# Optimization experiments

Hardware: AMD Instinct MI355X
Metric: run time of the kernel (lower is better)

The kernel has to match this reference:

```python
import jax, jax.numpy as jnp
import numpy as np
from jax import lax

BATCH = 2560
N_CLS = 128    # QP decision dim n
N_INEQ = 128   # number of inequality constraints
N_FEAT = 128
IPM_ITERS = 20
SIGMA = 0.1    # centering parameter


def setup_inputs() -> dict:
    key = jax.random.key(0)
    k1, k2, k3, k4, k5 = jax.random.split(key, 5)
    x = jax.random.normal(k1, (BATCH, N_FEAT), dtype=jnp.float32)
    # symmetric positive-definite Q (qpth requires PD Q)
    A = jax.random.normal(k2, (N_CLS, N_CLS), dtype=jnp.float32) / np.sqrt(N_CLS).astype(np.float32)
    Q = A @ A.T + 1e-4 * jnp.eye(N_CLS, dtype=jnp.float32)
    p = jax.random.normal(k3, (BATCH, N_CLS), dtype=jnp.float32)
    G = jax.random.uniform(k4, (N_INEQ, N_CLS), minval=-1.0, maxval=1.0, dtype=jnp.float32)
    # h > 0 so z = 0 is strictly feasible -> well-conditioned IPM
    h = jax.random.uniform(k5, (N_INEQ,), dtype=jnp.float32) + 1.0
    return {"x": x, "Q": Q, "p": p, "G": G, "h": h, "m": 1}


def _qp_solve(Q, p, G, h, iters=IPM_ITERS, sigma=SIGMA):
    """Batched primal-dual interior-point solve of
       min_z 1/2 z'Qz + p'z  s.t.  Gz + s = h, s >= 0.
    Q: [n,n] shared; p: [B,n]; G: [m,n] shared; h: [m] shared."""
    B, n = p.shape
    mI = G.shape[0]
    z = jnp.zeros((B, n), p.dtype)
    s = jnp.ones((B, mI), p.dtype)
    lam = jnp.ones((B, mI), p.dtype)
    GT = G.T

    def frac_to_boundary(v, dv):
        safe = jnp.where(dv < 0, dv, -1.0)
        r = jnp.where(dv < 0, -v / safe, 1e9)
        return jnp.minimum(1.0, 0.99 * jnp.min(r, axis=1, keepdims=True))

    def step(carry, _):
        z, s, lam = carry
        r_d = z @ Q.T + p + lam @ G          # [B,n]  Qz + p + G'lam
        r_p = z @ GT + s - h                 # [B,m]  Gz + s - h
        mu = jnp.mean(s * lam, axis=1, keepdims=True)
        r_c = s * lam - sigma * mu           # [B,m]
        d = lam / s                          # [B,m]
        # reduced KKT: (Q + G' D G) dz = -r_d + G'((r_c - lam*r_p)/s)
        M = Q[None] + jnp.einsum('ki,bk,kj->bij', G, d, G)  # [B,n,n]
        rhs = -r_d + ((r_c - lam * r_p) / s) @ G             # [B,n]
        dz = jnp.linalg.solve(M, rhs[..., None])[..., 0]
        ds = -r_p - dz @ GT
        dlam = (-r_c - lam * ds) / s
        a = jnp.minimum(frac_to_boundary(s, ds), frac_to_boundary(lam, dlam))
        return (z + a * dz, s + a * ds, lam + a * dlam), None

    (z, s, lam), _ = lax.scan(step, (z, s, lam), None, length=iters)
    return z


def reference(x, Q, p, G, h, m):
    # m==1 path of OptNet.forward: p stays [B,n], Q shared [n,n]
    pf = p.T if m > 1 else p
    z = _qp_solve(Q.astype(jnp.float32), pf.astype(jnp.float32),
                  G.astype(jnp.float32), h.astype(jnp.float32))
    out = z.reshape(10, -1)  # faithful to x.view(10, -1)
    return jax.nn.log_softmax(out, axis=1)
```

## Files before the change

kernel.cpp:

```cpp
#include <hip/hip_runtime.h>
#include <math.h>


#define B_TOT 2560
#define TB 32
#define NB (B_TOT/TB)

__device__ __forceinline__ int ROFF(int i){ return (i*(i+1))>>1; }
__device__ __forceinline__ int rowStart(int i){
  int a=i>>2, b=i&3;
  return ((a+1)*((a<<1)+b))<<2;
}
#define TRI_SZ 8448

__device__ __forceinline__ int rowOfIdx(int idx){
  int i = (int)((sqrtf(8.f*(float)idx+1.f)-1.f)*0.5f);
  while (((i+1)*(i+2)>>1) <= idx) ++i;
  while (((i*(i+1))>>1) > idx) --i;
  return i;
}

__device__ __forceinline__ void chol_diag_gj(float* tri, int c0, int lane){
  float rowA[16], rowW[16];
  const int r = lane;
  #pragma unroll
  for (int j=0;j<16;++j){ rowA[j]=0.f; rowW[j]=0.f; }
  if (r < 16){
    const float* src = &tri[rowStart(c0+r)+c0];
    #pragma unroll
    for (int q=0;q<4;++q){
      if (q <= (r>>2)){
        float4 w = *(const float4*)&src[4*q];
        rowA[4*q+0]=w.x; rowA[4*q+1]=w.y; rowA[4*q+2]=w.z; rowA[4*q+3]=w.w;
      }
    }
    #pragma unroll
    for (int j=0;j<16;++j) if (j>r) rowA[j]=0.f;
    #pragma unroll
    for (int j=0;j<16;++j) rowW[j] = (j==r)?1.f:0.f;
  }
  #pragma unroll
  for (int k=0;k<16;++k){
    float akk = __shfl(rowA[k], k, 64);
    akk = fmaxf(akk, 1e-12f);
    float linv = rsqrtf(akk);
    float lrk = rowA[k]*linv;
    if (r==k){
      #pragma unroll
      for (int c=0;c<16;++c) rowW[c] *= linv;
    }
    #pragma unroll
    for (int j=k+1;j<16;++j){
      float ljk = __shfl(lrk, j, 64);
      if (r>=j) rowA[j] = fmaf(-lrk, ljk, rowA[j]);
    }
    #pragma unroll
    for (int c=0;c<=k;++c){
      float wkc = __shfl(rowW[c], k, 64);
      if (r>k) rowW[c] = fmaf(-lrk, wkc, rowW[c]);
    }
  }
  if (r < 16){
    float* dst = &tri[rowStart(c0+r)+c0];
    #pragma unroll
    for (int q=0;q<4;++q){
      if (q <= (r>>2)){
        float4 w; w.x=rowW[4*q+0]; w.y=rowW[4*q+1]; w.z=rowW[4*q+2]; w.w=rowW[4*q+3];
        *(float4*)&dst[4*q] = w;
      }
    }
  }
}

__device__ __forceinline__ void trail_tile8(float* tri, int pc0, int i0, int j0,
                                            bool diag){
  float4 Pi[8][4], Pj[8][4];
  #pragma unroll
  for (int ii=0;ii<8;++ii){
    const float* rp = &tri[rowStart(i0+ii)+pc0];
    #pragma unroll
    for (int q=0;q<4;++q) Pi[ii][q] = *(const float4*)&rp[4*q];
  }
  #pragma unroll
  for (int jj=0;jj<8;++jj){
    const float* rp = &tri[rowStart(j0+jj)+pc0];
    #pragma unroll
    for (int q=0;q<4;++q) Pj[jj][q] = *(const float4*)&rp[4*q];
  }
  float acc[8][8];
  #pragma unroll
  for (int ii=0;ii<8;++ii)
    #pragma unroll
    for (int jj=0;jj<8;++jj) acc[ii][jj]=0.f;
  #pragma unroll
  for (int q=0;q<4;++q){
    #pragma unroll
    for (int ii=0;ii<8;++ii){
      #pragma unroll
      for (int jj=0;jj<8;++jj){
        acc[ii][jj] = fmaf(Pi[ii][q].x, Pj[jj][q].x, acc[ii][jj]);
        acc[ii][jj] = fmaf(Pi[ii][q].y, Pj[jj][q].y, acc[ii][jj]);
        acc[ii][jj] = fmaf(Pi[ii][q].z, Pj[jj][q].z, acc[ii][jj]);
        acc[ii][jj] = fmaf(Pi[ii][q].w, Pj[jj][q].w, acc[ii][jj]);
      }
    }
  }
  if (!diag){
    #pragma unroll
    for (int ii=0;ii<8;++ii){
      float4* p = (float4*)&tri[rowStart(i0+ii)+j0];
      float4 v0=p[0], v1=p[1];
      v0.x-=acc[ii][0]; v0.y-=acc[ii][1]; v0.z-=acc[ii][2]; v0.w-=acc[ii][3];
      v1.x-=acc[ii][4]; v1.y-=acc[ii][5]; v1.z-=acc[ii][6]; v1.w-=acc[ii][7];
      p[0]=v0; p[1]=v1;
    }
  } else {
    #pragma unroll
    for (int ii=0;ii<8;++ii){
      float4* p = (float4*)&tri[rowStart(i0+ii)+j0];
      const int nq = (ii>>2)+1;
      #pragma unroll
      for (int q=0;q<2;++q){
        if (q<nq){
          float4 v=p[q];
          v.x-=acc[ii][4*q+0]; v.y-=acc[ii][4*q+1];
          v.z-=acc[ii][4*q+2]; v.w-=acc[ii][4*q+3];
          p[q]=v;
        }
      }
    }
  }
}

__device__ __forceinline__ void trail_tile4(float* tri, int pc0, int i0, int j0){
  float4 Pi[4][4], Pj[4][4];
  #pragma unroll
  for (int ii=0;ii<4;++ii){
    const float* rp = &tri[rowStart(i0+ii)+pc0];
    #pragma unroll
    for (int q=0;q<4;++q) Pi[ii][q] = *(const float4*)&rp[4*q];
  }
  #pragma unroll
  for (int jj=0;jj<4;++jj){
    const float* rp = &tri[rowStart(j0+jj)+pc0];
    #pragma unroll
    for (int q=0;q<4;++q) Pj[jj][q] = *(const float4*)&rp[4*q];
  }
  float acc[4][4];
  #pragma unroll
  for (int ii=0;ii<4;++ii)
    #pragma unroll
    for (int jj=0;jj<4;++jj) acc[ii][jj]=0.f;
  #pragma unroll
  for (int q=0;q<4;++q){
    #pragma unroll
    for (int ii=0;ii<4;++ii){
      #pragma unroll
      for (int jj=0;jj<4;++jj){
        acc[ii][jj] = fmaf(Pi[ii][q].x, Pj[jj][q].x, acc[ii][jj]);
        acc[ii][jj] = fmaf(Pi[ii][q].y, Pj[jj][q].y, acc[ii][jj]);
        acc[ii][jj] = fmaf(Pi[ii][q].z, Pj[jj][q].z, acc[ii][jj]);
        acc[ii][jj] = fmaf(Pi[ii][q].w, Pj[jj][q].w, acc[ii][jj]);
      }
    }
  }
  #pragma unroll
  for (int ii=0;ii<4;++ii){
    float4* p = (float4*)&tri[rowStart(i0+ii)+j0];
    float4 v=p[0];
    v.x-=acc[ii][0]; v.y-=acc[ii][1]; v.z-=acc[ii][2]; v.w-=acc[ii][3];
    p[0]=v;
  }
}

__device__ __forceinline__ void panel_row(float* tri, int c0, int r){
  const int rb = rowStart(r)+c0;
  float a[16];
  #pragma unroll
  for (int q=0;q<4;++q){
    float4 w = *(const float4*)&tri[rb+4*q];
    a[4*q+0]=w.x; a[4*q+1]=w.y; a[4*q+2]=w.z; a[4*q+3]=w.w;
  }
  float x[16];
  #pragma unroll
  for (int c=0;c<16;++c){
    float acc=0.f;
    const int lb = rowStart(c0+c)+c0;
    #pragma unroll
    for (int q=0;q<=(c>>2);++q){
      float4 w = *(const float4*)&tri[lb+4*q];
      if (4*q+0<=c) acc = fmaf(w.x, a[4*q+0], acc);
      if (4*q+1<=c) acc = fmaf(w.y, a[4*q+1], acc);
      if (4*q+2<=c) acc = fmaf(w.z, a[4*q+2], acc);
      if (4*q+3<=c) acc = fmaf(w.w, a[4*q+3], acc);
    }
    x[c]=acc;
  }
  #pragma unroll
  for (int q=0;q<4;++q){
    float4 w; w.x=x[4*q+0]; w.y=x[4*q+1]; w.z=x[4*q+2]; w.w=x[4*q+3];
    *(float4*)&tri[rb+4*q] = w;
  }
}

__device__ void chol_factor(float* tri, int t, int lane, int wid){
  for (int kb=0; kb<8; ++kb){
    const int c0 = kb*16;
    if (wid==(kb&3)) chol_diag_gj(tri, c0, lane);
    __syncthreads();
    const int rem = 112 - c0;
    if (t < rem) panel_row(tri, c0, c0+16+t);
    __syncthreads();
    if (rem > 0){
      const int base = c0+16;
      const int T = rem>>3;
      const int ntile = (T*(T+1))>>1;
      for (int idx=t; idx<ntile; idx+=256){
        int I = rowOfIdx(idx);
        int J = idx - ROFF(I);
        trail_tile8(tri, c0, base+8*I, base+8*J, I==J);
      }
    }
    __syncthreads();
  }
}

__device__ void chol_factor_w2(float* tri, int t, int lane, int wid){
  for (int kb=0; kb<8; ++kb){
    const int c0 = kb*16;
    if (wid==0) chol_diag_gj(tri, c0, lane);
    __syncthreads();
    const int rem = 112 - c0;
    if (t < rem) panel_row(tri, c0, c0+16+t);
    __syncthreads();
    if (rem > 0){
      const int base = c0+16;
      const int R = rem>>2;
      const int ntile = (R*(R+1))>>1;
      for (int idx=t; idx<ntile; idx+=128){
        int I = rowOfIdx(idx);
        int J = idx - ROFF(I);
        trail_tile4(tri, c0, base+4*I, base+4*J);
      }
    }
    __syncthreads();
  }
}

__device__ void tri_solve_w2(const float* tri, float* rhs, int t){
  for (int kb=0;kb<8;++kb){
    const int c0=kb*16;
    if (t<16){
      const int c=t;
      const float* lrow = &tri[rowStart(c0+c)+c0];
      float acc=0.f;
      #pragma unroll
      for (int cp=0;cp<16;++cp) if (cp<=c) acc = fmaf(lrow[cp], rhs[c0+cp], acc);
      rhs[c0+c] = acc;
    }
    __syncthreads();
    const int rem = 112-c0;
    if (t<rem){
      const int r = c0+16+t;
      const int rb = rowStart(r)+c0;
      float acc = rhs[r];
      #pragma unroll
      for (int q=0;q<4;++q){
        float4 w = *(const float4*)&tri[rb+4*q];
        acc = fmaf(-w.x, rhs[c0+4*q+0], acc);
        acc = fmaf(-w.y, rhs[c0+4*q+1], acc);
        acc = fmaf(-w.z, rhs[c0+4*q+2], acc);
        acc = fmaf(-w.w, rhs[c0+4*q+3], acc);
      }
      rhs[r] = acc;
    }
    __syncthreads();
  }
  for (int kb=7;kb>=0;--kb){
    const int c0=kb*16;
    if (t<16){
      const int c=t;
      float acc=0.f;
      #pragma unroll
      for (int cp=0;cp<16;++cp)
        if (cp>=c) acc = fmaf(tri[rowStart(c0+cp)+c0+c], rhs[c0+cp], acc);
      rhs[c0+c] = acc;
    }
    __syncthreads();
    if (t<c0){
      float acc = rhs[t];
      #pragma unroll
      for (int c=0;c<16;++c) acc = fmaf(-tri[rowStart(c0+c)+t], rhs[c0+c], acc);
      rhs[t]=acc;
    }
    __syncthreads();
  }
}

__global__ __launch_bounds__(256) void k_prepA(const float* __restrict__ Q,
                                               float* __restrict__ TRIQ){
  __shared__ __align__(16) float tri[TRI_SZ];
  const int t = threadIdx.x;
  const int lane = t&63, wid = t>>6;
  for (int idx=t; idx<8256; idx+=256){
    int i = rowOfIdx(idx); int j = idx - ROFF(i);
    tri[rowStart(i)+j] = Q[i*128+j];
  }
  __syncthreads();
  chol_factor(tri, t, lane, wid);
  for (int idx=t; idx<TRI_SZ; idx+=256) TRIQ[idx]=tri[idx];
}

__global__ __launch_bounds__(256) void k_prepB(const float* __restrict__ TRIQ,
        const float* __restrict__ Gm, float* __restrict__ Qi, float* __restrict__ M1)
{
  __shared__ __align__(16) float tri[TRI_SZ];
  __shared__ float Xl[128*32];
  const int t = threadIdx.x, cc = blockIdx.x;
  const int a0 = (cc&3)*32;
  const bool ident = (cc<4);
  for (int idx=t; idx<TRI_SZ; idx+=256) tri[idx]=TRIQ[idx];
  for (int idx=t; idx<4096; idx+=256){
    int i=idx>>5, j=idx&31;
    Xl[idx] = ident ? ((i==(a0+j))?1.f:0.f) : Gm[(a0+j)*128+i];
  }
  __syncthreads();
  for (int kb=0;kb<8;++kb){
    const int c0=kb*16;
    if (t<32){
      float v[16], x[16];
      #pragma unroll
      for (int c=0;c<16;++c) v[c]=Xl[(c0+c)*32+t];
      #pragma unroll
      for (int c=0;c<16;++c){
        float acc=0.f;
        const int lb=rowStart(c0+c)+c0;
        #pragma unroll
        for (int cp=0;cp<16;++cp) if (cp<=c) acc=fmaf(tri[lb+cp], v[cp], acc);
        x[c]=acc;
      }
      #pragma unroll
      for (int c=0;c<16;++c) Xl[(c0+c)*32+t]=x[c];
    }
    __syncthreads();
    const int rem=112-c0;
    for (int rr=(t>>5); rr<rem; rr+=8){
      const int r=c0+16+rr, j=t&31;
      float acc=Xl[r*32+j];
      #pragma unroll
      for (int c=0;c<16;++c) acc = fmaf(-tri[rowStart(r)+c0+c], Xl[(c0+c)*32+j], acc);
      Xl[r*32+j]=acc;
    }
    __syncthreads();
  }
  for (int kb=7;kb>=0;--kb){
    const int c0=kb*16;
    if (t<32){
      float v[16], x[16];
      #pragma unroll
      for (int c=0;c<16;++c) v[c]=Xl[(c0+c)*32+t];
      #pragma unroll
      for (int c=0;c<16;++c){
        float acc=0.f;
        #pragma unroll
        for (int cp=0;cp<16;++cp) if (cp>=c) acc=fmaf(tri[rowStart(c0+cp)+c0+c], v[cp], acc);
        x[c]=acc;
      }
      #pragma unroll
      for (int c=0;c<16;++c) Xl[(c0+c)*32+t]=x[c];
    }
    __syncthreads();
    for (int rr=(t>>5); rr<c0; rr+=8){
      const int j=t&31;
      float acc=Xl[rr*32+j];
      #pragma unroll
      for (int c=0;c<16;++c) acc = fmaf(-tri[rowStart(c0+c)+rr], Xl[(c0+c)*32+j], acc);
      Xl[rr*32+j]=acc;
    }
    __syncthreads();
  }
  float* dst = ident ? Qi : M1;
  for (int idx=t; idx<4096; idx+=256){
    int i=idx>>5, j=idx&31;
    dst[i*128+a0+j] = Xl[idx];
  }
}

__global__ __launch_bounds__(256) void k_kmat(const float* __restrict__ Gm,
        const float* __restrict__ M1, float* __restrict__ K, float* __restrict__ Kd){
  const int idx = blockIdx.x*256 + threadIdx.x;
  const int a = idx>>7, bcol = idx&127;
  float a0=0.f,a1=0.f,a2=0.f,a3=0.f;
  #pragma unroll
  for (int j=0;j<128;j+=4){
    a0 = fmaf(Gm[a*128+j+0], M1[(j+0)*128+bcol], a0);
    a1 = fmaf(Gm[a*128+j+1], M1[(j+1)*128+bcol], a1);
    a2 = fmaf(Gm[a*128+j+2], M1[(j+2)*128+bcol], a2);
    a3 = fmaf(Gm[a*128+j+3], M1[(j+3)*128+bcol], a3);
  }
  float acc = (a0+a1)+(a2+a3);
  K[idx] = acc;
  if (a==bcol) Kd[a]=acc;
}

__global__ __launch_bounds__(256) void k_init(const float* __restrict__ p,
    float* __restrict__ Pt, float* __restrict__ S, float* __restrict__ LAM,
    float* __restrict__ GZ, float* __restrict__ QZ, float* __restrict__ Zst){
  int idx = blockIdx.x*256 + threadIdx.x;
  if (idx < 128*B_TOT){
    int i = idx/B_TOT, b = idx - i*B_TOT;
    Pt[idx] = p[b*128+i];
    S[idx]=1.f; LAM[idx]=1.f; GZ[idx]=0.f; QZ[idx]=0.f; Zst[idx]=0.f;
  }
}

__global__ __launch_bounds__(256) void k_B(const float* __restrict__ G,
    const float* __restrict__ M1, const float* __restrict__ Pt,
    const float* __restrict__ h,
    const float* __restrict__ S, const float* __restrict__ LAM,
    const float* __restrict__ GZ, const float* __restrict__ QZ,
    float* __restrict__ RHS, float* __restrict__ TV){
  __shared__ float wm_l[128*33];
  __shared__ float rhs_l[128*33];
  __shared__ float part_l[8*33];
  __shared__ float mu_l[TB];
  __shared__ float h_l[128];
  const int t=threadIdx.x, g=t>>5, bl=t&31;
  const int b = blockIdx.x*TB + bl;
  if (t<128) h_l[t]=h[t];
  __syncthreads();
  float sv[16], lv[16], rpv[16];
  float prod=0.f;
  #pragma unroll
  for (int q=0;q<16;++q){
    int i = g + 8*q;
    float s = S[i*B_TOT+b], l = LAM[i*B_TOT+b], gz = GZ[i*B_TOT+b];
    sv[q]=s; lv[q]=l; rpv[q]=gz+s-h_l[i];
    prod += s*l;
  }
  part_l[g*33+bl] = prod;
  __syncthreads();
  if (g==0){
    float m=0.f;
    #pragma unroll
    for (int q=0;q<8;++q) m += part_l[q*33+bl];
    mu_l[bl] = m*(1.f/128.f);
  }
  __syncthreads();
  const float mu = mu_l[bl];
  #pragma unroll
  for (int q=0;q<16;++q){
    int i=g+8*q;
    float rc = sv[q]*lv[q] - 0.1f*mu;
    wm_l[i*33+bl] = (rc - lv[q]*rpv[q])/sv[q] - lv[q];
  }
  __syncthreads();
  const int r0 = g*16;
  float acc[16];
  #pragma unroll
  for (int q=0;q<16;++q) acc[q] = -(QZ[(r0+q)*B_TOT+b] + Pt[(r0+q)*B_TOT+b]);
  #pragma unroll 2
  for (int j=0;j<128;++j){
    float wmv = wm_l[j*33+bl];
    const float4* gp = (const float4*)&G[j*128+r0];
    #pragma unroll
    for (int q4=0;q4<4;++q4){
      float4 gv = gp[q4];
      acc[4*q4+0]=fmaf(gv.x,wmv,acc[4*q4+0]);
      acc[4*q4+1]=fmaf(gv.y,wmv,acc[4*q4+1]);
      acc[4*q4+2]=fmaf(gv.z,wmv,acc[4*q4+2]);
      acc[4*q4+3]=fmaf(gv.w,wmv,acc[4*q4+3]);
    }
  }
  #pragma unroll
  for (int q=0;q<16;++q){
    rhs_l[(r0+q)*33+bl]=acc[q];
    RHS[(r0+q)*B_TOT+b]=acc[q];
  }
  __syncthreads();
  #pragma unroll
  for (int q=0;q<16;++q) acc[q]=0.f;
  #pragma unroll 2
  for (int j=0;j<128;++j){
    float rv = rhs_l[j*33+bl];
    const float4* mp = (const float4*)&M1[j*128+r0];
    #pragma unroll
    for (int q4=0;q4<4;++q4){
      float4 mv = mp[q4];
      acc[4*q4+0]=fmaf(mv.x,rv,acc[4*q4+0]);
      acc[4*q4+1]=fmaf(mv.y,rv,acc[4*q4+1]);
      acc[4*q4+2]=fmaf(mv.z,rv,acc[4*q4+2]);
      acc[4*q4+3]=fmaf(mv.w,rv,acc[4*q4+3]);
    }
  }
  #pragma unroll
  for (int q=0;q<16;++q) TV[(r0+q)*B_TOT+b]=acc[q];
}

__global__ __launch_bounds__(128) void k_C(const float* __restrict__ K,
    const float* __restrict__ Kd, const float* __restrict__ h,
    const float* __restrict__ TV,
    float* __restrict__ S, float* __restrict__ LAM, float* __restrict__ GZ,
    float* __restrict__ Y, float* __restrict__ ALPHA){
  __shared__ __align__(16) float tri[TRI_SZ];
  __shared__ float scl_l[128];
  __shared__ float sh_t[128];
  __shared__ float red[2];
  const int t = threadIdx.x, b = blockIdx.x;
  const int lane = t&63, wid = t>>6;
  float s_t=S[t*B_TOT+b], l_t=LAM[t*B_TOT+b], g_t=GZ[t*B_TOT+b];
  float rp_t = g_t + s_t - h[t];
  float prod = s_t*l_t;
  #pragma unroll
  for (int o=32;o>0;o>>=1) prod += __shfl_xor(prod,o,64);
  if (lane==0) red[wid]=prod;
  __syncthreads();
  const float mu = (red[0]+red[1])*(1.f/128.f);
  float rc_t = s_t*l_t - 0.1f*mu;
  float di_t = fminf(s_t/l_t, 1e30f);
  float sc_t = rsqrtf(Kd[t]+di_t);
  scl_l[t]=sc_t;
  sh_t[t]=TV[t*B_TOT+b]*sc_t;
  __syncthreads();
  #pragma unroll 4
  for (int i=0;i<128;++i){
    if (t<=i) tri[rowStart(i)+t] = (t==i)?1.f : K[i*128+t]*scl_l[i]*sc_t;
  }
  __syncthreads();
  chol_factor_w2(tri, t, lane, wid);
  tri_solve_w2(tri, sh_t, t);
  float y = sh_t[t]*sc_t;
  float gd = di_t*y;
  float ds = -rp_t - gd;
  float dl = (-rc_t - l_t*ds)/s_t;
  float ra = 1e9f;
  if (ds<0.f) ra = -s_t/ds;
  if (dl<0.f) ra = fminf(ra,-l_t/dl);
  #pragma unroll
  for (int o=32;o>0;o>>=1) ra = fminf(ra,__shfl_xor(ra,o,64));
  __syncthreads();
  if (lane==0) red[wid]=ra;
  __syncthreads();
  const float alpha = fminf(1.0f, 0.99f*fminf(red[0],red[1]));
  S[t*B_TOT+b]   = s_t + alpha*ds;
  LAM[t*B_TOT+b] = l_t + alpha*dl;
  GZ[t*B_TOT+b]  = g_t + alpha*gd;
  Y[t*B_TOT+b]   = y;
  if (t==0) ALPHA[b]=alpha;
}

__global__ __launch_bounds__(256) void k_DB(const float* __restrict__ G,
    const float* __restrict__ Qi, const float* __restrict__ M1,
    const float* __restrict__ Pt, const float* __restrict__ h,
    const float* __restrict__ S, const float* __restrict__ LAM,
    const float* __restrict__ GZ,
    const float* __restrict__ Y, const float* __restrict__ ALPHA,
    float* __restrict__ Zst, float* __restrict__ QZ,
    float* __restrict__ RHS, float* __restrict__ TV){
  __shared__ float bufA[128*33];
  __shared__ float bufB[128*33];
  __shared__ float part_l[8*33];
  __shared__ float mu_l[TB];
  __shared__ float h_l[128];
  const int t=threadIdx.x, g=t>>5, bl=t&31;
  const int b = blockIdx.x*TB + bl;
  const int r0 = g*16;
  if (t<128) h_l[t]=h[t];
  #pragma unroll
  for (int q=0;q<16;++q){
    int i=g+8*q;
    bufA[i*33+bl] = Y[i*B_TOT+b];
  }
  const float alpha = ALPHA[b];
  __syncthreads();
  float acc[16];
  #pragma unroll
  for (int q=0;q<16;++q) acc[q]=RHS[(r0+q)*B_TOT+b];
  #pragma unroll 2
  for (int j=0;j<128;++j){
    float yv = bufA[j*33+bl];
    const float4* gp=(const float4*)&G[j*128+r0];
    #pragma unroll
    for (int q4=0;q4<4;++q4){
      float4 gv=gp[q4];
      acc[4*q4+0]=fmaf(-gv.x,yv,acc[4*q4+0]);
      acc[4*q4+1]=fmaf(-gv.y,yv,acc[4*q4+1]);
      acc[4*q4+2]=fmaf(-gv.z,yv,acc[4*q4+2]);
      acc[4*q4+3]=fmaf(-gv.w,yv,acc[4*q4+3]);
    }
  }
  __syncthreads();
  #pragma unroll
  for (int q=0;q<16;++q){
    const int i=r0+q;
    float qz_new = QZ[i*B_TOT+b] + alpha*acc[q];
    QZ[i*B_TOT+b] = qz_new;
    bufB[i*33+bl] = acc[q];
    bufA[i*33+bl] = qz_new;
  }
  __syncthreads();
  #pragma unroll
  for (int q=0;q<16;++q) acc[q]=0.f;
  #pragma unroll 2
  for (int j=0;j<128;++j){
    float vv = bufB[j*33+bl];
    const float4* qp4=(const float4*)&Qi[j*128+r0];
    #pragma unroll
    for (int q4=0;q4<4;++q4){
      float4 qv=qp4[q4];
      acc[4*q4+0]=fmaf(qv.x,vv,acc[4*q4+0]);
      acc[4*q4+1]=fmaf(qv.y,vv,acc[4*q4+1]);
      acc[4*q4+2]=fmaf(qv.z,vv,acc[4*q4+2]);
      acc[4*q4+3]=fmaf(qv.w,vv,acc[4*q4+3]);
    }
  }
  #pragma unroll
  for (int q=0;q<16;++q){
    float* zp=&Zst[(r0+q)*B_TOT+b];
    *zp = *zp + alpha*acc[q];
  }
  __syncthreads();
  float sv[16], lv[16], rpv[16];
  float prod=0.f;
  #pragma unroll
  for (int q=0;q<16;++q){
    int i = g + 8*q;
    float s = S[i*B_TOT+b], l = LAM[i*B_TOT+b], gz = GZ[i*B_TOT+b];
    sv[q]=s; lv[q]=l; rpv[q]=gz+s-h_l[i];
    prod += s*l;
  }
  part_l[g*33+bl] = prod;
  __syncthreads();
  if (g==0){
    float m=0.f;
    #pragma unroll
    for (int q=0;q<8;++q) m += part_l[q*33+bl];
    mu_l[bl] = m*(1.f/128.f);
  }
  __syncthreads();
  const float mu = mu_l[bl];
  #pragma unroll
  for (int q=0;q<16;++q){
    int i=g+8*q;
    float rc = sv[q]*lv[q] - 0.1f*mu;
    bufB[i*33+bl] = (rc - lv[q]*rpv[q])/sv[q] - lv[q];
  }
  __syncthreads();
  #pragma unroll
  for (int q=0;q<16;++q) acc[q] = -(bufA[(r0+q)*33+bl] + Pt[(r0+q)*B_TOT+b]);
  #pragma unroll 2
  for (int j=0;j<128;++j){
    float wmv = bufB[j*33+bl];
    const float4* gp = (const float4*)&G[j*128+r0];
    #pragma unroll
    for (int q4=0;q4<4;++q4){
      float4 gv = gp[q4];
      acc[4*q4+0]=fmaf(gv.x,wmv,acc[4*q4+0]);
      acc[4*q4+1]=fmaf(gv.y,wmv,acc[4*q4+1]);
      acc[4*q4+2]=fmaf(gv.z,wmv,acc[4*q4+2]);
      acc[4*q4+3]=fmaf(gv.w,wmv,acc[4*q4+3]);
    }
  }
  __syncthreads();
  #pragma unroll
  for (int q=0;q<16;++q){
    RHS[(r0+q)*B_TOT+b]=acc[q];
    bufA[(r0+q)*33+bl]=acc[q];
  }
  __syncthreads();
  #pragma unroll
  for (int q=0;q<16;++q) acc[q]=0.f;
  #pragma unroll 2
  for (int j=0;j<128;++j){
    float rv = bufA[j*33+bl];
    const float4* mp = (const float4*)&M1[j*128+r0];
    #pragma unroll
    for (int q4=0;q4<4;++q4){
      float4 mv = mp[q4];
      acc[4*q4+0]=fmaf(mv.x,rv,acc[4*q4+0]);
      acc[4*q4+1]=fmaf(mv.y,rv,acc[4*q4+1]);
      acc[4*q4+2]=fmaf(mv.z,rv,acc[4*q4+2]);
      acc[4*q4+3]=fmaf(mv.w,rv,acc[4*q4+3]);
    }
  }
  #pragma unroll
  for (int q=0;q<16;++q) TV[(r0+q)*B_TOT+b]=acc[q];
}

__global__ __launch_bounds__(256) void k_D(const float* __restrict__ G,
    const float* __restrict__ Qi, const float* __restrict__ RHS,
    const float* __restrict__ Y, const float* __restrict__ ALPHA,
    float* __restrict__ Zst, float* __restrict__ QZ){
  __shared__ float y_l[128*33];
  __shared__ float v_l[128*33];
  const int t=threadIdx.x, g=t>>5, bl=t&31;
  const int b = blockIdx.x*TB + bl;
  #pragma unroll
  for (int q=0;q<16;++q){
    int i=g+8*q;
    y_l[i*33+bl] = Y[i*B_TOT+b];
  }
  const float alpha = ALPHA[b];
  __syncthreads();
  const int r0=g*16;
  float acc[16];
  #pragma unroll
  for (int q=0;q<16;++q) acc[q]=RHS[(r0+q)*B_TOT+b];
  #pragma unroll 2
  for (int j=0;j<128;++j){
    float yv = y_l[j*33+bl];
    const float4* gp=(const float4*)&G[j*128+r0];
    #pragma unroll
    for (int q4=0;q4<4;++q4){
      float4 gv=gp[q4];
      acc[4*q4+0]=fmaf(-gv.x,yv,acc[4*q4+0]);
      acc[4*q4+1]=fmaf(-gv.y,yv,acc[4*q4+1]);
      acc[4*q4+2]=fmaf(-gv.z,yv,acc[4*q4+2]);
      acc[4*q4+3]=fmaf(-gv.w,yv,acc[4*q4+3]);
    }
  }
  #pragma unroll
  for (int q=0;q<16;++q){
    v_l[(r0+q)*33+bl]=acc[q];
    float* qp=&QZ[(r0+q)*B_TOT+b];
    *qp = *qp + alpha*acc[q];
  }
  __syncthreads();
  #pragma unroll
  for (int q=0;q<16;++q) acc[q]=0.f;
  #pragma unroll 2
  for (int j=0;j<128;++j){
    float vv = v_l[j*33+bl];
    const float4* qp4=(const float4*)&Qi[j*128+r0];
    #pragma unroll
    for (int q4=0;q4<4;++q4){
      float4 qv=qp4[q4];
      acc[4*q4+0]=fmaf(qv.x,vv,acc[4*q4+0]);
      acc[4*q4+1]=fmaf(qv.y,vv,acc[4*q4+1]);
      acc[4*q4+2]=fmaf(qv.z,vv,acc[4*q4+2]);
      acc[4*q4+3]=fmaf(qv.w,vv,acc[4*q4+3]);
    }
  }
  #pragma unroll
  for (int q=0;q<16;++q){
    float* zp=&Zst[(r0+q)*B_TOT+b];
    *zp = *zp + alpha*acc[q];
  }
}

__global__ __launch_bounds__(1024) void k_logsoftmax(const float* __restrict__ Zst,
                                                     float* __restrict__ out){
  __shared__ float red[16];
  __shared__ float sval[2];
  const int r = blockIdx.x, t = threadIdx.x;
  float m = -1e30f;
  for (int k=t;k<32768;k+=1024){
    float v = Zst[(k&127)*B_TOT + r*256 + (k>>7)];
    m = fmaxf(m, v);
  }
  #pragma unroll
  for (int o=32;o>0;o>>=1) m = fmaxf(m, __shfl_down(m,o,64));
  if ((t&63)==0) red[t>>6] = m;
  __syncthreads();
  if (t==0){ float mm=red[0]; for (int w=1;w<16;++w) mm=fmaxf(mm,red[w]); sval[0]=mm; }
  __syncthreads();
  const float mx = sval[0];
  float s=0.f;
  for (int k=t;k<32768;k+=1024){
    float v = Zst[(k&127)*B_TOT + r*256 + (k>>7)];
    s += expf(v-mx);
  }
  #pragma unroll
  for (int o=32;o>0;o>>=1) s += __shfl_down(s,o,64);
  if ((t&63)==0) red[t>>6]=s;
  __syncthreads();
  if (t==0){ float ss=0.f; for (int w=0;w<16;++w) ss+=red[w]; sval[1]=logf(ss); }
  __syncthreads();
  const float lse = sval[1];
  for (int k=t;k<32768;k+=1024){
    float v = Zst[(k&127)*B_TOT + r*256 + (k>>7)];
    out[(size_t)r*32768+k] = v-mx-lse;
  }
}

extern "C" void kernel_launch(void* const* d_in, const int* in_sizes, int n_in,
                              void* d_out, int out_size, void* d_ws, size_t ws_size,
                              hipStream_t stream){
  const float* Q = (const float*)d_in[1];
  const float* p = (const float*)d_in[2];
  const float* G = (const float*)d_in[3];
  const float* h = (const float*)d_in[4];
  float* ws  = (float*)d_ws;
  const int NE = 128*B_TOT;
  float* Zst = ws;
  float* Qi  = Zst + NE;
  float* M1  = Qi + 16384;
  float* K   = M1 + 16384;
  float* Kd  = K + 16384;
  float* ALPHA = Kd + 128;
  float* Pt  = ALPHA + 2560;
  float* S   = Pt + NE;
  float* LAM = S + NE;
  float* GZ  = LAM + NE;
  float* QZ  = GZ + NE;
  float* RHS = QZ + NE;
  float* TV  = RHS + NE;
  float* Y   = TV + NE;
  float* TRIQ= Y + NE;
  float* out = (float*)d_out;

  hipLaunchKernelGGL(k_prepA, dim3(1), dim3(256), 0, stream, Q, TRIQ);
  hipLaunchKernelGGL(k_prepB, dim3(8), dim3(256), 0, stream, TRIQ, G, Qi, M1);
  hipLaunchKernelGGL(k_kmat, dim3(64), dim3(256), 0, stream, G, M1, K, Kd);
  hipLaunchKernelGGL(k_init, dim3((NE+255)/256), dim3(256), 0, stream,
                     p, Pt, S, LAM, GZ, QZ, Zst);
  hipLaunchKernelGGL(k_B, dim3(NB), dim3(256), 0, stream,
                     G, M1, Pt, h, S, LAM, GZ, QZ, RHS, TV);
  for (int it=0; it<20; ++it){
    hipLaunchKernelGGL(k_C, dim3(B_TOT), dim3(128), 0, stream,
                       K, Kd, h, TV, S, LAM, GZ, Y, ALPHA);
    if (it < 19){
      hipLaunchKernelGGL(k_DB, dim3(NB), dim3(256), 0, stream,
                         G, Qi, M1, Pt, h, S, LAM, GZ, Y, ALPHA,
                         Zst, QZ, RHS, TV);
    } else {
      hipLaunchKernelGGL(k_D, dim3(NB), dim3(256), 0, stream,
                         G, Qi, RHS, Y, ALPHA, Zst, QZ);
    }
  }
  hipLaunchKernelGGL(k_logsoftmax, dim3(10), dim3(1024), 0, stream, Zst, out);
}
```

Measured before the change: 8.089 ms.

## Use 192 threads in Cholesky kernel with contiguous tile ranges and Pi reuse

```diff
diff --git a/kernel.cpp b/kernel.cpp
--- a/kernel.cpp
+++ b/kernel.cpp
@@ -5,6 +5,7 @@
 #define B_TOT 2560
 #define TB 32
 #define NB (B_TOT/TB)
+#define NTC 192
 
 __device__ __forceinline__ int ROFF(int i){ return (i*(i+1))>>1; }
 __device__ __forceinline__ int rowStart(int i){
@@ -132,14 +133,10 @@
   }
 }
 
-__device__ __forceinline__ void trail_tile4(float* tri, int pc0, int i0, int j0){
-  float4 Pi[4][4], Pj[4][4];
-  #pragma unroll
-  for (int ii=0;ii<4;++ii){
-    const float* rp = &tri[rowStart(i0+ii)+pc0];
-    #pragma unroll
-    for (int q=0;q<4;++q) Pi[ii][q] = *(const float4*)&rp[4*q];
-  }
+__device__ __forceinline__ void trail_tile4_pi(float* tri, int pc0,
+                                               const float4 Pi[4][4],
+                                               int i0, int j0){
+  float4 Pj[4][4];
   #pragma unroll
   for (int jj=0;jj<4;++jj){
     const float* rp = &tri[rowStart(j0+jj)+pc0];
@@ -170,6 +167,16 @@
     float4 v=p[0];
     v.x-=acc[ii][0]; v.y-=acc[ii][1]; v.z-=acc[ii][2]; v.w-=acc[ii][3];
     p[0]=v;
+  }
+}
+
+__device__ __forceinline__ void load_pi4(const float* tri, int pc0, int i0,
+                                         float4 Pi[4][4]){
+  #pragma unroll
+  for (int ii=0;ii<4;++ii){
+    const float* rp = &tri[rowStart(i0+ii)+pc0];
+    #pragma unroll
+    for (int q=0;q<4;++q) Pi[ii][q] = *(const float4*)&rp[4*q];
   }
 }
 
@@ -225,7 +232,7 @@
   }
 }
 
-__device__ void chol_factor_w2(float* tri, int t, int lane, int wid){
+__device__ void chol_factor_w3(float* tri, int t, int lane, int wid){
   for (int kb=0; kb<8; ++kb){
     const int c0 = kb*16;
     if (wid==0) chol_diag_gj(tri, c0, lane);
@@ -235,12 +242,25 @@
     __syncthreads();
     if (rem > 0){
       const int base = c0+16;
-      const int R = rem>>2;
-      const int ntile = (R*(R+1))>>1;
-      for (int idx=t; idx<ntile; idx+=128){
-        int I = rowOfIdx(idx);
-        int J = idx - ROFF(I);
-        trail_tile4(tri, c0, base+4*I, base+4*J);
+      const int T = rem>>2;
+      const int ntile = (T*(T+1))>>1;
+      const int lo = (ntile*t)/NTC;
+      const int hi = (ntile*(t+1))/NTC;
+      if (lo < hi){
+        int I = rowOfIdx(lo);
+        int nextRow = ROFF(I+1);
+        float4 Pi[4][4];
+        load_pi4(tri, c0, base+4*I, Pi);
+        for (int idx=lo; idx<hi; ++idx){
+          if (idx >= nextRow){
+            ++I;
+            while (idx >= ROFF(I+1)) ++I;
+            nextRow = ROFF(I+1);
+            load_pi4(tri, c0, base+4*I, Pi);
+          }
+          const int J = idx - ROFF(I);
+          trail_tile4_pi(tri, c0, Pi, base+4*I, base+4*J);
+        }
       }
     }
     __syncthreads();
@@ -497,7 +517,7 @@
   for (int q=0;q<16;++q) TV[(r0+q)*B_TOT+b]=acc[q];
 }
 
-__global__ __launch_bounds__(128) void k_C(const float* __restrict__ K,
+__global__ __launch_bounds__(NTC) void k_C(const float* __restrict__ K,
     const float* __restrict__ Kd, const float* __restrict__ h,
     const float* __restrict__ TV,
     float* __restrict__ S, float* __restrict__ LAM, float* __restrict__ GZ,
@@ -505,47 +525,59 @@
   __shared__ __align__(16) float tri[TRI_SZ];
   __shared__ float scl_l[128];
   __shared__ float sh_t[128];
-  __shared__ float red[2];
+  __shared__ float red[3];
   const int t = threadIdx.x, b = blockIdx.x;
   const int lane = t&63, wid = t>>6;
-  float s_t=S[t*B_TOT+b], l_t=LAM[t*B_TOT+b], g_t=GZ[t*B_TOT+b];
-  float rp_t = g_t + s_t - h[t];
-  float prod = s_t*l_t;
+  float s_t=0.f,l_t=0.f,g_t=0.f,rp_t=0.f;
+  float prod = 0.f;
+  if (t<128){
+    s_t=S[t*B_TOT+b]; l_t=LAM[t*B_TOT+b]; g_t=GZ[t*B_TOT+b];
+    rp_t = g_t + s_t - h[t];
+    prod = s_t*l_t;
+  }
   #pragma unroll
   for (int o=32;o>0;o>>=1) prod += __shfl_xor(prod,o,64);
   if (lane==0) red[wid]=prod;
   __syncthreads();
-  const float mu = (red[0]+red[1])*(1.f/128.f);
-  float rc_t = s_t*l_t - 0.1f*mu;
-  float di_t = fminf(s_t/l_t, 1e30f);
-  float sc_t = rsqrtf(Kd[t]+di_t);
-  scl_l[t]=sc_t;
-  sh_t[t]=TV[t*B_TOT+b]*sc_t;
+  const float mu = (red[0]+red[1]+red[2])*(1.f/128.f);
+  float rc_t=0.f, di_t=0.f, sc_t=0.f;
+  if (t<128){
+    rc_t = s_t*l_t - 0.1f*mu;
+    di_t = fminf(s_t/l_t, 1e30f);
+    sc_t = rsqrtf(Kd[t]+di_t);
+    scl_l[t]=sc_t;
+    sh_t[t]=TV[t*B_TOT+b]*sc_t;
+  }
   __syncthreads();
   #pragma unroll 4
   for (int i=0;i<128;++i){
     if (t<=i) tri[rowStart(i)+t] = (t==i)?1.f : K[i*128+t]*scl_l[i]*sc_t;
   }
   __syncthreads();
-  chol_factor_w2(tri, t, lane, wid);
+  chol_factor_w3(tri, t, lane, wid);
   tri_solve_w2(tri, sh_t, t);
-  float y = sh_t[t]*sc_t;
-  float gd = di_t*y;
-  float ds = -rp_t - gd;
-  float dl = (-rc_t - l_t*ds)/s_t;
+  float y=0.f, gd=0.f, ds=0.f, dl=0.f;
   float ra = 1e9f;
-  if (ds<0.f) ra = -s_t/ds;
-  if (dl<0.f) ra = fminf(ra,-l_t/dl);
+  if (t<128){
+    y = sh_t[t]*sc_t;
+    gd = di_t*y;
+    ds = -rp_t - gd;
+    dl = (-rc_t - l_t*ds)/s_t;
+    if (ds<0.f) ra = -s_t/ds;
+    if (dl<0.f) ra = fminf(ra,-l_t/dl);
+  }
   #pragma unroll
   for (int o=32;o>0;o>>=1) ra = fminf(ra,__shfl_xor(ra,o,64));
   __syncthreads();
   if (lane==0) red[wid]=ra;
   __syncthreads();
-  const float alpha = fminf(1.0f, 0.99f*fminf(red[0],red[1]));
-  S[t*B_TOT+b]   = s_t + alpha*ds;
-  LAM[t*B_TOT+b] = l_t + alpha*dl;
-  GZ[t*B_TOT+b]  = g_t + alpha*gd;
-  Y[t*B_TOT+b]   = y;
+  const float alpha = fminf(1.0f, 0.99f*fminf(fminf(red[0],red[1]),red[2]));
+  if (t<128){
+    S[t*B_TOT+b]   = s_t + alpha*ds;
+    LAM[t*B_TOT+b] = l_t + alpha*dl;
+    GZ[t*B_TOT+b]  = g_t + alpha*gd;
+    Y[t*B_TOT+b]   = y;
+  }
   if (t==0) ALPHA[b]=alpha;
 }
 
@@ -817,7 +849,7 @@
   hipLaunchKernelGGL(k_B, dim3(NB), dim3(256), 0, stream,
                      G, M1, Pt, h, S, LAM, GZ, QZ, RHS, TV);
   for (int it=0; it<20; ++it){
-    hipLaunchKernelGGL(k_C, dim3(B_TOT), dim3(128), 0, stream,
+    hipLaunchKernelGGL(k_C, dim3(B_TOT), dim3(NTC), 0, stream,
                        K, Kd, h, TV, S, LAM, GZ, Y, ALPHA);
     if (it < 19){
       hipLaunchKernelGGL(k_DB, dim3(NB), dim3(256), 0, stream,
```

Result: slower. 10.89 ms (+34.7%).

## Shrink k_DB/k_D batch tile to 8 to raise block count

Applied to the files above, without the earlier changes.

```diff
diff --git a/kernel.cpp b/kernel.cpp
--- a/kernel.cpp
+++ b/kernel.cpp
@@ -5,6 +5,8 @@
 #define B_TOT 2560
 #define TB 32
 #define NB (B_TOT/TB)
+#define TBD 8
+#define NBD (B_TOT/TBD)
 
 __device__ __forceinline__ int ROFF(int i){ return (i*(i+1))>>1; }
 __device__ __forceinline__ int rowStart(int i){
@@ -557,192 +559,163 @@
     const float* __restrict__ Y, const float* __restrict__ ALPHA,
     float* __restrict__ Zst, float* __restrict__ QZ,
     float* __restrict__ RHS, float* __restrict__ TV){
-  __shared__ float bufA[128*33];
-  __shared__ float bufB[128*33];
-  __shared__ float part_l[8*33];
-  __shared__ float mu_l[TB];
+  __shared__ float bufA[128*9];
+  __shared__ float bufB[128*9];
+  __shared__ float part_l[32*9];
+  __shared__ float mu_l[TBD];
   __shared__ float h_l[128];
-  const int t=threadIdx.x, g=t>>5, bl=t&31;
-  const int b = blockIdx.x*TB + bl;
-  const int r0 = g*16;
+  const int t=threadIdx.x, g=t>>3, bl=t&7;
+  const int b = blockIdx.x*TBD + bl;
+  const int r0 = g*4;
   if (t<128) h_l[t]=h[t];
   #pragma unroll
-  for (int q=0;q<16;++q){
-    int i=g+8*q;
-    bufA[i*33+bl] = Y[i*B_TOT+b];
-  }
+  for (int q=0;q<4;++q) bufA[(r0+q)*9+bl] = Y[(r0+q)*B_TOT+b];
   const float alpha = ALPHA[b];
   __syncthreads();
-  float acc[16];
-  #pragma unroll
-  for (int q=0;q<16;++q) acc[q]=RHS[(r0+q)*B_TOT+b];
-  #pragma unroll 2
+  float acc[4];
+  #pragma unroll
+  for (int q=0;q<4;++q) acc[q]=RHS[(r0+q)*B_TOT+b];
+  #pragma unroll 4
   for (int j=0;j<128;++j){
-    float yv = bufA[j*33+bl];
-    const float4* gp=(const float4*)&G[j*128+r0];
-    #pragma unroll
-    for (int q4=0;q4<4;++q4){
-      float4 gv=gp[q4];
-      acc[4*q4+0]=fmaf(-gv.x,yv,acc[4*q4+0]);
-      acc[4*q4+1]=fmaf(-gv.y,yv,acc[4*q4+1]);
-      acc[4*q4+2]=fmaf(-gv.z,yv,acc[4*q4+2]);
-      acc[4*q4+3]=fmaf(-gv.w,yv,acc[4*q4+3]);
-    }
-  }
-  __syncthreads();
-  #pragma unroll
-  for (int q=0;q<16;++q){
+    float yv = bufA[j*9+bl];
+    float4 gv = *(const float4*)&G[j*128+r0];
+    acc[0]=fmaf(-gv.x,yv,acc[0]);
+    acc[1]=fmaf(-gv.y,yv,acc[1]);
+    acc[2]=fmaf(-gv.z,yv,acc[2]);
+    acc[3]=fmaf(-gv.w,yv,acc[3]);
+  }
+  __syncthreads();
+  #pragma unroll
+  for (int q=0;q<4;++q){
     const int i=r0+q;
     float qz_new = QZ[i*B_TOT+b] + alpha*acc[q];
     QZ[i*B_TOT+b] = qz_new;
-    bufB[i*33+bl] = acc[q];
-    bufA[i*33+bl] = qz_new;
-  }
-  __syncthreads();
-  #pragma unroll
-  for (int q=0;q<16;++q) acc[q]=0.f;
-  #pragma unroll 2
+    bufB[i*9+bl] = acc[q];
+    bufA[i*9+bl] = qz_new;
+  }
+  __syncthreads();
+  #pragma unroll
+  for (int q=0;q<4;++q) acc[q]=0.f;
+  #pragma unroll 4
   for (int j=0;j<128;++j){
-    float vv = bufB[j*33+bl];
-    const float4* qp4=(const float4*)&Qi[j*128+r0];
-    #pragma unroll
-    for (int q4=0;q4<4;++q4){
-      float4 qv=qp4[q4];
-      acc[4*q4+0]=fmaf(qv.x,vv,acc[4*q4+0]);
-      acc[4*q4+1]=fmaf(qv.y,vv,acc[4*q4+1]);
-      acc[4*q4+2]=fmaf(qv.z,vv,acc[4*q4+2]);
-      acc[4*q4+3]=fmaf(qv.w,vv,acc[4*q4+3]);
-    }
-  }
-  #pragma unroll
-  for (int q=0;q<16;++q){
+    float vv = bufB[j*9+bl];
+    float4 qv = *(const float4*)&Qi[j*128+r0];
+    acc[0]=fmaf(qv.x,vv,acc[0]);
+    acc[1]=fmaf(qv.y,vv,acc[1]);
+    acc[2]=fmaf(qv.z,vv,acc[2]);
+    acc[3]=fmaf(qv.w,vv,acc[3]);
+  }
+  #pragma unroll
+  for (int q=0;q<4;++q){
     float* zp=&Zst[(r0+q)*B_TOT+b];
     *zp = *zp + alpha*acc[q];
   }
   __syncthreads();
-  float sv[16], lv[16], rpv[16];
+  float sv[4], lv[4], rpv[4];
   float prod=0.f;
   #pragma unroll
-  for (int q=0;q<16;++q){
-    int i = g + 8*q;
+  for (int q=0;q<4;++q){
+    const int i=r0+q;
     float s = S[i*B_TOT+b], l = LAM[i*B_TOT+b], gz = GZ[i*B_TOT+b];
     sv[q]=s; lv[q]=l; rpv[q]=gz+s-h_l[i];
     prod += s*l;
   }
-  part_l[g*33+bl] = prod;
-  __syncthreads();
-  if (g==0){
+  part_l[g*9+bl] = prod;
+  __syncthreads();
+  if (t<TBD){
     float m=0.f;
     #pragma unroll
-    for (int q=0;q<8;++q) m += part_l[q*33+bl];
-    mu_l[bl] = m*(1.f/128.f);
+    for (int r=0;r<32;++r) m += part_l[r*9+t];
+    mu_l[t] = m*(1.f/128.f);
   }
   __syncthreads();
   const float mu = mu_l[bl];
   #pragma unroll
-  for (int q=0;q<16;++q){
-    int i=g+8*q;
+  for (int q=0;q<4;++q){
+    const int i=r0+q;
     float rc = sv[q]*lv[q] - 0.1f*mu;
-    bufB[i*33+bl] = (rc - lv[q]*rpv[q])/sv[q] - lv[q];
-  }
-  __syncthreads();
-  #pragma unroll
-  for (int q=0;q<16;++q) acc[q] = -(bufA[(r0+q)*33+bl] + Pt[(r0+q)*B_TOT+b]);
-  #pragma unroll 2
+    bufB[i*9+bl] = (rc - lv[q]*rpv[q])/sv[q] - lv[q];
+  }
+  __syncthreads();
+  #pragma unroll
+  for (int q=0;q<4;++q) acc[q] = -(bufA[(r0+q)*9+bl] + Pt[(r0+q)*B_TOT+b]);
+  #pragma unroll 4
   for (int j=0;j<128;++j){
-    float wmv = bufB[j*33+bl];
-    const float4* gp = (const float4*)&G[j*128+r0];
-    #pragma unroll
-    for (int q4=0;q4<4;++q4){
-      float4 gv = gp[q4];
-      acc[4*q4+0]=fmaf(gv.x,wmv,acc[4*q4+0]);
-      acc[4*q4+1]=fmaf(gv.y,wmv,acc[4*q4+1]);
-      acc[4*q4+2]=fmaf(gv.z,wmv,acc[4*q4+2]);
-      acc[4*q4+3]=fmaf(gv.w,wmv,acc[4*q4+3]);
-    }
-  }
-  __syncthreads();
-  #pragma unroll
-  for (int q=0;q<16;++q){
+    float wmv = bufB[j*9+bl];
+    float4 gv = *(const float4*)&G[j*128+r0];
+    acc[0]=fmaf(gv.x,wmv,acc[0]);
+    acc[1]=fmaf(gv.y,wmv,acc[1]);
+    acc[2]=fmaf(gv.z,wmv,acc[2]);
+    acc[3]=fmaf(gv.w,wmv,acc[3]);
+  }
+  __syncthreads();
+  #pragma unroll
+  for (int q=0;q<4;++q){
     RHS[(r0+q)*B_TOT+b]=acc[q];
-    bufA[(r0+q)*33+bl]=acc[q];
-  }
-  __syncthreads();
-  #pragma unroll
-  for (int q=0;q<16;++q) acc[q]=0.f;
-  #pragma unroll 2
+    bufA[(r0+q)*9+bl]=acc[q];
+  }
+  __syncthreads();
+  #pragma unroll
+  for (int q=0;q<4;++q) acc[q]=0.f;
+  #pragma unroll 4
   for (int j=0;j<128;++j){
-    float rv = bufA[j*33+bl];
-    const float4* mp = (const float4*)&M1[j*128+r0];
-    #pragma unroll
-    for (int q4=0;q4<4;++q4){
-      float4 mv = mp[q4];
-      acc[4*q4+0]=fmaf(mv.x,rv,acc[4*q4+0]);
-      acc[4*q4+1]=fmaf(mv.y,rv,acc[4*q4+1]);
-      acc[4*q4+2]=fmaf(mv.z,rv,acc[4*q4+2]);
-      acc[4*q4+3]=fmaf(mv.w,rv,acc[4*q4+3]);
-    }
-  }
-  #pragma unroll
-  for (int q=0;q<16;++q) TV[(r0+q)*B_TOT+b]=acc[q];
+    float rv = bufA[j*9+bl];
+    float4 mv = *(const float4*)&M1[j*128+r0];
+    acc[0]=fmaf(mv.x,rv,acc[0]);
+    acc[1]=fmaf(mv.y,rv,acc[1]);
+    acc[2]=fmaf(mv.z,rv,acc[2]);
+    acc[3]=fmaf(mv.w,rv,acc[3]);
+  }
+  #pragma unroll
+  for (int q=0;q<4;++q) TV[(r0+q)*B_TOT+b]=acc[q];
 }
 
 __global__ __launch_bounds__(256) void k_D(const float* __restrict__ G,
     const float* __restrict__ Qi, const float* __restrict__ RHS,
     const float* __restrict__ Y, const float* __restrict__ ALPHA,
     float* __restrict__ Zst, float* __restrict__ QZ){
-  __shared__ float y_l[128*33];
-  __shared__ float v_l[128*33];
-  const int t=threadIdx.x, g=t>>5, bl=t&31;
-  const int b = blockIdx.x*TB + bl;
-  #pragma unroll
-  for (int q=0;q<16;++q){
-    int i=g+8*q;
-    y_l[i*33+bl] = Y[i*B_TOT+b];
-  }
+  __shared__ float y_l[128*9];
+  __shared__ float v_l[128*9];
+  const int t=threadIdx.x, g=t>>3, bl=t&7;
+  const int b = blockIdx.x*TBD + bl;
+  const int r0 = g*4;
+  #pragma unroll
+  for (int q=0;q<4;++q) y_l[(r0+q)*9+bl] = Y[(r0+q)*B_TOT+b];
   const float alpha = ALPHA[b];
   __syncthreads();
-  const int r0=g*16;
-  float acc[16];
-  #pragma unroll
-  for (int q=0;q<16;++q) acc[q]=RHS[(r0+q)*B_TOT+b];
-  #pragma unroll 2
+  float acc[4];
+  #pragma unroll
+  for (int q=0;q<4;++q) acc[q]=RHS[(r0+q)*B_TOT+b];
+  #pragma unroll 4
   for (int j=0;j<128;++j){
-    float yv = y_l[j*33+bl];
-    const float4* gp=(const float4*)&G[j*128+r0];
-    #pragma unroll
-    for (int q4=0;q4<4;++q4){
-      float4 gv=gp[q4];
-      acc[4*q4+0]=fmaf(-gv.x,yv,acc[4*q4+0]);
-      acc[4*q4+1]=fmaf(-gv.y,yv,acc[4*q4+1]);
-      acc[4*q4+2]=fmaf(-gv.z,yv,acc[4*q4+2]);
-      acc[4*q4+3]=fmaf(-gv.w,yv,acc[4*q4+3]);
-    }
-  }
-  #pragma unroll
-  for (int q=0;q<16;++q){
-    v_l[(r0+q)*33+bl]=acc[q];
-    float* qp=&QZ[(r0+q)*B_TOT+b];
+    float yv = y_l[j*9+bl];
+    float4 gv = *(const float4*)&G[j*128+r0];
+    acc[0]=fmaf(-gv.x,yv,acc[0]);
+    acc[1]=fmaf(-gv.y,yv,acc[1]);
+    acc[2]=fmaf(-gv.z,yv,acc[2]);
+    acc[3]=fmaf(-gv.w,yv,acc[3]);
+  }
+  #pragma unroll
+  for (int q=0;q<4;++q){
+    const int i=r0+q;
+    v_l[i*9+bl]=acc[q];
+    float* qp=&QZ[i*B_TOT+b];
     *qp = *qp + alpha*acc[q];
   }
   __syncthreads();
   #pragma unroll
-  for (int q=0;q<16;++q) acc[q]=0.f;
-  #pragma unroll 2
+  for (int q=0;q<4;++q) acc[q]=0.f;
+  #pragma unroll 4
   for (int j=0;j<128;++j){
-    float vv = v_l[j*33+bl];
-    const float4* qp4=(const float4*)&Qi[j*128+r0];
-    #pragma unroll
-    for (int q4=0;q4<4;++q4){
-      float4 qv=qp4[q4];
-      acc[4*q4+0]=fmaf(qv.x,vv,acc[4*q4+0]);
-      acc[4*q4+1]=fmaf(qv.y,vv,acc[4*q4+1]);
-      acc[4*q4+2]=fmaf(qv.z,vv,acc[4*q4+2]);
-      acc[4*q4+3]=fmaf(qv.w,vv,acc[4*q4+3]);
-    }
-  }
-  #pragma unroll
-  for (int q=0;q<16;++q){
+    float vv = v_l[j*9+bl];
+    float4 qv = *(const float4*)&Qi[j*128+r0];
+    acc[0]=fmaf(qv.x,vv,acc[0]);
+    acc[1]=fmaf(qv.y,vv,acc[1]);
+    acc[2]=fmaf(qv.z,vv,acc[2]);
+    acc[3]=fmaf(qv.w,vv,acc[3]);
+  }
+  #pragma unroll
+  for (int q=0;q<4;++q){
     float* zp=&Zst[(r0+q)*B_TOT+b];
     *zp = *zp + alpha*acc[q];
   }
@@ -820,11 +793,11 @@
     hipLaunchKernelGGL(k_C, dim3(B_TOT), dim3(128), 0, stream,
                        K, Kd, h, TV, S, LAM, GZ, Y, ALPHA);
     if (it < 19){
-      hipLaunchKernelGGL(k_DB, dim3(NB), dim3(256), 0, stream,
+      hipLaunchKernelGGL(k_DB, dim3(NBD), dim3(256), 0, stream,
                          G, Qi, M1, Pt, h, S, LAM, GZ, Y, ALPHA,
                          Zst, QZ, RHS, TV);
     } else {
-      hipLaunchKernelGGL(k_D, dim3(NB), dim3(256), 0, stream,
+      hipLaunchKernelGGL(k_D, dim3(NBD), dim3(256), 0, stream,
                          G, Qi, RHS, Y, ALPHA, Zst, QZ);
     }
   }
```

After: 7.338 ms. 1.1x faster.
